# Kernel tuning notes

Measured on AMD Instinct MI355X. Metric: run time of the kernel, lower is better.

Reference implementation:

```python
import jax, jax.numpy as jnp
import numpy as np

EMBED_DIM = 1024
NUM_HEADS = 16
HEAD_DIM = EMBED_DIM // NUM_HEADS
SCALING = HEAD_DIM ** -0.5
TGT_LEN, BSZ = 2048, 2


def setup_inputs() -> dict:
    key = jax.random.key(0)
    k1, k2, k3 = jax.random.split(key, 3)
    return {
        "query": jax.random.normal(k1, (TGT_LEN, BSZ, EMBED_DIM), jnp.float32),
        "in_proj_weight": jax.random.normal(k2, (3 * EMBED_DIM, EMBED_DIM), jnp.float32) * (EMBED_DIM ** -0.5),
        "in_proj_bias": jnp.zeros((3 * EMBED_DIM,), jnp.float32),
        "out_w": jax.random.normal(k3, (EMBED_DIM, EMBED_DIM), jnp.float32) * (EMBED_DIM ** -0.5),
        "out_b": jnp.zeros((EMBED_DIM,), jnp.float32),
    }


def reference(query, in_proj_weight, in_proj_bias, out_w, out_b):
    tgt_len, bsz, embed_dim = query.shape
    # fused QKV projection (self-attention path: qkv_same)
    qkv = query @ in_proj_weight.T + in_proj_bias  # [T, B, 3E]
    q, k, v = jnp.split(qkv, 3, axis=-1)
    q = q * SCALING
    # [T, B, E] -> [B*H, T, hd]
    def to_heads(x):
        return x.reshape(tgt_len, bsz * NUM_HEADS, HEAD_DIM).transpose(1, 0, 2)
    q, k, v = to_heads(q), to_heads(k), to_heads(v)
    attn_weights = jnp.einsum('bqd,bkd->bqk', q, k)          # [B*H, T, T]
    attn_weights = jax.nn.softmax(attn_weights, axis=-1)
    attn = jnp.einsum('bqk,bkd->bqd', attn_weights, v)       # [B*H, T, hd]
    attn = attn.transpose(1, 0, 2).reshape(tgt_len, bsz, embed_dim)
    attn = attn @ out_w.T + out_b
    # averaged attention weights over heads (need_weights=True)
    avg_weights = attn_weights.reshape(bsz, NUM_HEADS, tgt_len, tgt_len).mean(axis=1)
    return attn, avg_weights
```

## Files before the change

kernel.cpp:

```cpp
#include <hip/hip_runtime.h>
#include <hip/hip_bf16.h>
#include <math.h>

#define T_LEN 2048
#define BSZ   2
#define EMB   1024
#define NH    16
#define HD    64
#define BHN   (BSZ*NH)
#define M1    (T_LEN*BSZ)
#define SCAL  0.125f
#define QSCALE (0.125f * 1.44269504088896f)

typedef __attribute__((ext_vector_type(8))) short bf16x8;
typedef __attribute__((ext_vector_type(4))) float f32x4;
typedef __attribute__((ext_vector_type(2))) unsigned int u32x2;

__device__ inline unsigned short f2bf(float x) {
    union { float f; unsigned u; } v; v.f = x;
    unsigned r = v.u + 0x7FFF + ((v.u >> 16) & 1);
    return (unsigned short)(r >> 16);
}

__device__ inline unsigned pack2bf(float a, float b) {
    union { __hip_bfloat162 h; unsigned u; } v;
    v.h = __float22bfloat162_rn(make_float2(a, b));
    return v.u;
}

__device__ inline float fexp2(float x) {
#if __has_builtin(__builtin_amdgcn_exp2f)
    return __builtin_amdgcn_exp2f(x);
#else
    return exp2f(x);
#endif
}

__device__ inline void async16(const unsigned short* g, unsigned short* l) {
    __builtin_amdgcn_global_load_lds(
        (const __attribute__((address_space(1))) void*)g,
        (__attribute__((address_space(3))) void*)l, 16, 0, 0);
}

__device__ inline void bar() {
    asm volatile("" ::: "memory");
    __builtin_amdgcn_s_barrier();
    asm volatile("" ::: "memory");
}

__device__ inline unsigned short* swz(unsigned short* base, int r, int c) {
    return base + (((r << 3) + (c ^ (r & 7))) << 3);
}
__device__ inline const unsigned short* swz(const unsigned short* base, int r, int c) {
    return base + (((r << 3) + (c ^ (r & 7))) << 3);
}

__device__ inline void xchg(unsigned e, unsigned o, unsigned& w_lo, unsigned& w_hi) {
#if __has_builtin(__builtin_amdgcn_permlane32_swap) && __has_builtin(__builtin_amdgcn_permlane16_swap)
    u32x2 x = __builtin_amdgcn_permlane32_swap(e, o, false, false);
    u32x2 y = __builtin_amdgcn_permlane16_swap(x[0], x[1], false, false);
    w_lo = y[0]; w_hi = y[1];
#else
    int lane = (int)(threadIdx.x & 63);
    int quad = lane >> 4, l16 = lane & 15;
    int srcA = ((quad & 1) * 2) * 16 + l16;
    int srcB = ((quad & 1) * 2 + 1) * 16 + l16;
    unsigned ea = (unsigned)__shfl((int)e, srcA, 64);
    unsigned oa = (unsigned)__shfl((int)o, srcA, 64);
    unsigned eb = (unsigned)__shfl((int)e, srcB, 64);
    unsigned ob = (unsigned)__shfl((int)o, srcB, 64);
    w_lo = (quad >> 1) ? oa : ea;
    w_hi = (quad >> 1) ? ob : eb;
#endif
}

__global__ __launch_bounds__(256) void cvt3_kernel(
    const float* __restrict__ s0, const float* __restrict__ s1,
    const float* __restrict__ s2, unsigned short* __restrict__ dst,
    int n0, int n1)
{
    int idx = blockIdx.x * 256 + threadIdx.x;
    const float* src; int o;
    if (idx < n0)           { src = s0; o = idx; }
    else if (idx < n0 + n1) { src = s1; o = idx - n0; }
    else                    { src = s2; o = idx - n0 - n1; }
    float4 a = reinterpret_cast<const float4*>(src)[(size_t)o * 2];
    float4 c = reinterpret_cast<const float4*>(src)[(size_t)o * 2 + 1];
    unsigned w[4] = { pack2bf(a.x, a.y), pack2bf(a.z, a.w),
                      pack2bf(c.x, c.y), pack2bf(c.z, c.w) };
    reinterpret_cast<uint4*>(dst)[idx] = *reinterpret_cast<uint4*>(w);
}

__global__ __launch_bounds__(256) void qkv_mfma_kernel(
    const unsigned short* __restrict__ A, const unsigned short* __restrict__ B,
    const float* __restrict__ bias,
    unsigned short* __restrict__ Q16, unsigned short* __restrict__ K16,
    unsigned short* __restrict__ Vt16)
{
    constexpr int BM = 128, BN = 128, BK = 32, K = 1024;
    __shared__ unsigned short As[BM * BK];
    __shared__ unsigned short Bs[BN * BK];
    const int tid = threadIdx.x;
    const int lane = tid & 63, wave = tid >> 6;
    const int quad = lane >> 4, l16 = lane & 15;
    const int wr = wave >> 1, wc = wave & 1;
    const int m0 = blockIdx.x * BM, n0 = blockIdx.y * BN;

    f32x4 zero4 = {0.f, 0.f, 0.f, 0.f};
    f32x4 acc[4][4];
    #pragma unroll
    for (int i = 0; i < 4; ++i)
        #pragma unroll
        for (int j = 0; j < 4; ++j) acc[i][j] = zero4;

    for (int k0 = 0; k0 < K; k0 += BK) {
        __syncthreads();
        #pragma unroll
        for (int t = 0; t < 2; ++t) {
            int c = t * 256 + tid;
            int m = c >> 2, kb = c & 3;
            async16(&A[(size_t)(m0 + m) * K + k0 + kb * 8], &As[c * 8]);
            async16(&B[(size_t)(n0 + m) * K + k0 + kb * 8], &Bs[c * 8]);
        }
        __syncthreads();
        bf16x8 af[4], bfr[4];
        #pragma unroll
        for (int i = 0; i < 4; ++i) {
            af[i]  = *reinterpret_cast<const bf16x8*>(&As[(wr * 64 + i * 16 + l16) * BK + quad * 8]);
            bfr[i] = *reinterpret_cast<const bf16x8*>(&Bs[(wc * 64 + i * 16 + l16) * BK + quad * 8]);
        }
        #pragma unroll
        for (int i = 0; i < 4; ++i)
            #pragma unroll
            for (int j = 0; j < 4; ++j)
                acc[i][j] = __builtin_amdgcn_mfma_f32_16x16x32_bf16(af[i], bfr[j], acc[i][j], 0, 0, 0);
    }

    #pragma unroll
    for (int j = 0; j < 4; ++j) {
        int n = n0 + wc * 64 + j * 16 + l16;
        float bv = bias[n];
        int which = n >> 10;
        int c = n & 1023;
        int h = c >> 6, d = c & 63;
        #pragma unroll
        for (int i = 0; i < 4; ++i) {
            #pragma unroll
            for (int r = 0; r < 4; ++r) {
                int m = m0 + wr * 64 + i * 16 + quad * 4 + r;
                int t = m >> 1, b = m & 1;
                int bh = b * NH + h;
                float v = acc[i][j][r] + bv;
                if (which == 0)      Q16[((size_t)bh * T_LEN + t) * HD + d] = f2bf(v * QSCALE);
                else if (which == 1) K16[((size_t)bh * T_LEN + t) * HD + d] = f2bf(v);
                else                 Vt16[((size_t)bh * HD + d) * T_LEN + t] = f2bf(v);
            }
        }
    }
}

__global__ __launch_bounds__(512, 4) void flash_mfma_kernel(
    const unsigned short* __restrict__ Qb, const unsigned short* __restrict__ Kb,
    const unsigned short* __restrict__ Vt, unsigned short* __restrict__ AO,
    float* __restrict__ Rrow)
{
    __shared__ unsigned short Ks[2][64 * 64];
    __shared__ unsigned short Vs[2][64 * 64];
    const int tid = threadIdx.x;
    const int lane = tid & 63, wave = tid >> 6;
    const int quad = lane >> 4, l16 = lane & 15;

    const int lin = blockIdx.y * gridDim.x + blockIdx.x;
    const int xcd = lin & 7, slot = lin >> 3;
    const int bh = xcd * 4 + (slot >> 4);
    const int qt = slot & 15;
    const int q0 = qt * 128;
    const int b = bh >> 4, h = bh & 15;

    const unsigned short* Qp =
        Qb + ((size_t)bh * T_LEN + q0 + wave * 16 + l16) * HD;
    bf16x8 qf0 = *reinterpret_cast<const bf16x8*>(Qp + quad * 8);
    bf16x8 qf1 = *reinterpret_cast<const bf16x8*>(Qp + 32 + quad * 8);

    f32x4 zero4 = {0.f, 0.f, 0.f, 0.f};
    f32x4 oacc[4] = {zero4, zero4, zero4, zero4};
    float l_part = 0.f;

    const unsigned short* Kbase = Kb + (size_t)bh * T_LEN * HD;
    const unsigned short* Vbase = Vt + (size_t)bh * HD * T_LEN;

    const int r0 = tid >> 3, c0 = (tid & 7) ^ (r0 & 7);

    async16(&Kbase[(size_t)r0 * HD + c0 * 8], &Ks[0][tid * 8]);
    async16(&Vbase[(size_t)r0 * T_LEN + c0 * 8], &Vs[0][tid * 8]);

    int cur = 0;
    for (int kt = 0; kt < T_LEN; kt += 64) {
        if (kt + 64 < T_LEN) {
            const int nb = cur ^ 1, nkt = kt + 64;
            async16(&Kbase[(size_t)(nkt + r0) * HD + c0 * 8], &Ks[nb][tid * 8]);
            async16(&Vbase[(size_t)r0 * T_LEN + nkt + c0 * 8], &Vs[nb][tid * 8]);
            asm volatile("s_waitcnt vmcnt(2)" ::: "memory");
        } else {
            asm volatile("s_waitcnt vmcnt(0)" ::: "memory");
        }
        bar();

        const unsigned short* Kt = Ks[cur];
        const unsigned short* Vv = Vs[cur];

        f32x4 sacc[4] = {zero4, zero4, zero4, zero4};
        __builtin_amdgcn_s_setprio(1);
        #pragma unroll
        for (int kb = 0; kb < 4; ++kb) {
            bf16x8 kf0 = *reinterpret_cast<const bf16x8*>(swz(Kt, kb * 16 + l16, quad));
            sacc[kb] = __builtin_amdgcn_mfma_f32_16x16x32_bf16(kf0, qf0, sacc[kb], 0, 0, 0);
            bf16x8 kf1 = *reinterpret_cast<const bf16x8*>(swz(Kt, kb * 16 + l16, 4 + quad));
            sacc[kb] = __builtin_amdgcn_mfma_f32_16x16x32_bf16(kf1, qf1, sacc[kb], 0, 0, 0);
        }
        __builtin_amdgcn_s_setprio(0);

        unsigned dlo[4], dhi[4];
        #pragma unroll
        for (int kb = 0; kb < 4; ++kb) {
            float p0 = fexp2(sacc[kb][0]);
            float p1 = fexp2(sacc[kb][1]);
            float p2 = fexp2(sacc[kb][2]);
            float p3 = fexp2(sacc[kb][3]);
            l_part += (p0 + p1) + (p2 + p3);
            dlo[kb] = pack2bf(p0, p1);
            dhi[kb] = pack2bf(p2, p3);
        }

        bf16x8 pfrag[2];
        #pragma unroll
        for (int ks = 0; ks < 2; ++ks) {
            unsigned w0, w1, w2, w3;
            xchg(dlo[2 * ks], dlo[2 * ks + 1], w0, w2);
            xchg(dhi[2 * ks], dhi[2 * ks + 1], w1, w3);
            union { bf16x8 v; unsigned u[4]; } P;
            P.u[0] = w0; P.u[1] = w1; P.u[2] = w2; P.u[3] = w3;
            pfrag[ks] = P.v;
        }

        __builtin_amdgcn_s_setprio(1);
        #pragma unroll
        for (int ks = 0; ks < 2; ++ks) {
            #pragma unroll
            for (int dt = 0; dt < 4; ++dt) {
                bf16x8 va = *reinterpret_cast<const bf16x8*>(swz(Vv, dt * 16 + l16, ks * 4 + quad));
                oacc[dt] = __builtin_amdgcn_mfma_f32_16x16x32_bf16(va, pfrag[ks], oacc[dt], 0, 0, 0);
            }
        }
        __builtin_amdgcn_s_setprio(0);

        bar();
        cur ^= 1;
    }

    l_part += __shfl_xor(l_part, 16);
    l_part += __shfl_xor(l_part, 32);
    float rl = 1.0f / l_part;
    int q = q0 + wave * 16 + l16;
    size_t base = ((size_t)q * BSZ + b) * EMB + h * HD;
    #pragma unroll
    for (int dt = 0; dt < 4; ++dt) {
        unsigned o[2] = { pack2bf(oacc[dt][0] * rl, oacc[dt][1] * rl),
                          pack2bf(oacc[dt][2] * rl, oacc[dt][3] * rl) };
        *reinterpret_cast<uint2*>(&AO[base + dt * 16 + quad * 4]) = *reinterpret_cast<uint2*>(o);
    }
    if (quad == 0)
        Rrow[(size_t)bh * T_LEN + q] = rl;
}

__global__ __launch_bounds__(256) void avg_mfma_kernel(
    const unsigned short* __restrict__ Qb, const unsigned short* __restrict__ Kb,
    const float* __restrict__ Rrow, float* __restrict__ avg_out)
{
    __shared__ unsigned short Ks[2][2][64 * 64];
    const int tid = threadIdx.x;
    const int lane = tid & 63, wave = tid >> 6;
    const int quad = lane >> 4, l16 = lane & 15;
    const int kt = blockIdx.x, qt = blockIdx.y, b = blockIdx.z;
    const int q0 = qt * 128, k0 = kt * 64;

    auto stage_pair = [&](int buf, int h0) {
        const unsigned short* Kg = Kb + ((size_t)(b * NH + h0) * T_LEN + k0) * HD;
        #pragma unroll
        for (int t = 0; t < 4; ++t) {
            int c = t * 256 + tid;
            int hh = c >> 9, cl = c & 511;
            int r = cl >> 3, cc = (cl & 7) ^ (r & 7);
            async16(&Kg[(size_t)hh * T_LEN * HD + (size_t)r * HD + cc * 8],
                    &Ks[buf][0][0] + (size_t)c * 8);
        }
    };

    f32x4 zero4 = {0.f, 0.f, 0.f, 0.f};
    f32x4 acc[2][4];
    #pragma unroll
    for (int s = 0; s < 2; ++s)
        #pragma unroll
        for (int c = 0; c < 4; ++c) acc[s][c] = zero4;

    stage_pair(0, 0);
    int cur = 0;
    for (int g = 0; g < NH / 2; ++g) {
        if (g + 1 < NH / 2) {
            stage_pair(cur ^ 1, 2 * (g + 1));
            asm volatile("s_waitcnt vmcnt(4)" ::: "memory");
        } else {
            asm volatile("s_waitcnt vmcnt(0)" ::: "memory");
        }
        bar();

        #pragma unroll
        for (int hh = 0; hh < 2; ++hh) {
            const int bh = b * NH + 2 * g + hh;
            const unsigned short* Kt = Ks[cur][hh];
            bf16x8 kf[4][2];
            #pragma unroll
            for (int c = 0; c < 4; ++c) {
                kf[c][0] = *reinterpret_cast<const bf16x8*>(swz(Kt, c * 16 + l16, quad));
                kf[c][1] = *reinterpret_cast<const bf16x8*>(swz(Kt, c * 16 + l16, 4 + quad));
            }
            #pragma unroll
            for (int s = 0; s < 2; ++s) {
                const int qrow = q0 + s * 64 + wave * 16;
                const unsigned short* Qp = Qb + ((size_t)bh * T_LEN + qrow + l16) * HD;
                bf16x8 qf0 = *reinterpret_cast<const bf16x8*>(Qp + quad * 8);
                bf16x8 qf1 = *reinterpret_cast<const bf16x8*>(Qp + 32 + quad * 8);
                float4 rlv = *reinterpret_cast<const float4*>(
                    &Rrow[(size_t)bh * T_LEN + qrow + quad * 4]);

                f32x4 sacc[4] = {zero4, zero4, zero4, zero4};
                __builtin_amdgcn_s_setprio(1);
                #pragma unroll
                for (int c = 0; c < 4; ++c) {
                    sacc[c] = __builtin_amdgcn_mfma_f32_16x16x32_bf16(qf0, kf[c][0], sacc[c], 0, 0, 0);
                    sacc[c] = __builtin_amdgcn_mfma_f32_16x16x32_bf16(qf1, kf[c][1], sacc[c], 0, 0, 0);
                }
                __builtin_amdgcn_s_setprio(0);

                float rl4[4] = { rlv.x, rlv.y, rlv.z, rlv.w };
                #pragma unroll
                for (int c = 0; c < 4; ++c)
                    #pragma unroll
                    for (int r = 0; r < 4; ++r)
                        acc[s][c][r] += fexp2(sacc[c][r]) * rl4[r];
            }
        }
        bar();
        cur ^= 1;
    }

    #pragma unroll
    for (int s = 0; s < 2; ++s)
        #pragma unroll
        for (int r = 0; r < 4; ++r) {
            int q = q0 + s * 64 + wave * 16 + quad * 4 + r;
            size_t base = ((size_t)b * T_LEN + q) * T_LEN + k0;
            #pragma unroll
            for (int c = 0; c < 4; ++c)
                avg_out[base + c * 16 + l16] = acc[s][c][r] * (1.0f / 16.0f);
        }
}

__global__ __launch_bounds__(256) void out_mfma_kernel(
    const unsigned short* __restrict__ A, const unsigned short* __restrict__ B,
    const float* __restrict__ bias, float* __restrict__ out)
{
    constexpr int BM = 128, BN = 128, BK = 32, K = 1024;
    __shared__ unsigned short As[BM * BK];
    __shared__ unsigned short Bs[BN * BK];
    const int tid = threadIdx.x;
    const int lane = tid & 63, wave = tid >> 6;
    const int quad = lane >> 4, l16 = lane & 15;
    const int wr = wave >> 1, wc = wave & 1;
    const int m0 = blockIdx.x * BM, n0 = blockIdx.y * BN;

    f32x4 zero4 = {0.f, 0.f, 0.f, 0.f};
    f32x4 acc[4][4];
    #pragma unroll
    for (int i = 0; i < 4; ++i)
        #pragma unroll
        for (int j = 0; j < 4; ++j) acc[i][j] = zero4;

    for (int k0 = 0; k0 < K; k0 += BK) {
        __syncthreads();
        #pragma unroll
        for (int t = 0; t < 2; ++t) {
            int c = t * 256 + tid;
            int m = c >> 2, kb = c & 3;
            async16(&A[(size_t)(m0 + m) * K + k0 + kb * 8], &As[c * 8]);
            async16(&B[(size_t)(n0 + m) * K + k0 + kb * 8], &Bs[c * 8]);
        }
        __syncthreads();
        bf16x8 af[4], bfr[4];
        #pragma unroll
        for (int i = 0; i < 4; ++i) {
            af[i]  = *reinterpret_cast<const bf16x8*>(&As[(wr * 64 + i * 16 + l16) * BK + quad * 8]);
            bfr[i] = *reinterpret_cast<const bf16x8*>(&Bs[(wc * 64 + i * 16 + l16) * BK + quad * 8]);
        }
        #pragma unroll
        for (int i = 0; i < 4; ++i)
            #pragma unroll
            for (int j = 0; j < 4; ++j)
                acc[i][j] = __builtin_amdgcn_mfma_f32_16x16x32_bf16(af[i], bfr[j], acc[i][j], 0, 0, 0);
    }

    #pragma unroll
    for (int j = 0; j < 4; ++j) {
        int n = n0 + wc * 64 + j * 16 + l16;
        float bv = bias[n];
        #pragma unroll
        for (int i = 0; i < 4; ++i) {
            #pragma unroll
            for (int r = 0; r < 4; ++r) {
                int m = m0 + wr * 64 + i * 16 + quad * 4 + r;
                out[(size_t)m * 1024 + n] = acc[i][j][r] + bv;
            }
        }
    }
}

extern "C" void kernel_launch(void* const* d_in, const int* in_sizes, int n_in,
                              void* d_out, int out_size, void* d_ws, size_t ws_size,
                              hipStream_t stream)
{
    const float* query = (const float*)d_in[0];
    const float* wqkv  = (const float*)d_in[1];
    const float* bqkv  = (const float*)d_in[2];
    const float* wout  = (const float*)d_in[3];
    const float* bout  = (const float*)d_in[4];
    float* out = (float*)d_out;

    char* ws = (char*)d_ws;
    const size_t E_Q   = (size_t)M1 * EMB;
    const size_t E_W   = (size_t)3 * EMB * EMB;
    const size_t E_WO  = (size_t)EMB * EMB;
    const size_t E_QKV = (size_t)BHN * T_LEN * HD;

    unsigned short* queryb = (unsigned short*)ws;
    unsigned short* wqkvb  = queryb + E_Q;
    unsigned short* woutb  = wqkvb + E_W;
    unsigned short* Q16    = woutb + E_WO;
    unsigned short* K16    = Q16 + E_QKV;
    unsigned short* Vt16   = K16 + E_QKV;
    unsigned short* AO16   = Vt16 + E_QKV;
    float* Lr = (float*)(AO16 + E_Q);
    const size_t need = (E_Q + E_W + E_WO + 4 * E_QKV) * 2 + (size_t)BHN * T_LEN * 4;
    if (ws_size < need) return;

    cvt3_kernel<<<(int)((E_Q + E_W + E_WO) / 8 / 256), 256, 0, stream>>>(
        query, wqkv, wout, queryb, (int)(E_Q / 8), (int)(E_W / 8));

    qkv_mfma_kernel<<<dim3(M1 / 128, 3072 / 128), 256, 0, stream>>>(queryb, wqkvb, bqkv, Q16, K16, Vt16);
    flash_mfma_kernel<<<dim3(T_LEN / 128, BHN), 512, 0, stream>>>(Q16, K16, Vt16, AO16, Lr);
    avg_mfma_kernel<<<dim3(T_LEN / 64, T_LEN / 128, BSZ), 256, 0, stream>>>(Q16, K16, Lr, out + (size_t)M1 * EMB);
    out_mfma_kernel<<<dim3(M1 / 128, 1024 / 128), 256, 0, stream>>>(AO16, woutb, bout, out);
}
```

Measured before the change: 242.3 us.

## Double K/V tile size in flash kernel and restructure avg kernel to 512 threads

The flash attention kernel now stages 128-key K and V tiles per iteration instead of 64, which halves the number of barriers and loop iterations and adds a 16-chunk swizzle for the wider V tile. The averaged-weights kernel moves to 512 threads with 128-key tiles. Each wave now owns 16 query rows across 8 key blocks instead of 32 rows across 4 blocks, so K fragments are read per pass rather than reused for two query sub-tiles. LDS use doubles in both kernels, which can lower occupancy, and register pressure rises from the wider score and accumulator arrays.

```diff
diff --git a/kernel.cpp b/kernel.cpp
--- a/kernel.cpp
+++ b/kernel.cpp
@@ -48,11 +48,11 @@
     asm volatile("" ::: "memory");
 }
 
-__device__ inline unsigned short* swz(unsigned short* base, int r, int c) {
-    return base + (((r << 3) + (c ^ (r & 7))) << 3);
-}
 __device__ inline const unsigned short* swz(const unsigned short* base, int r, int c) {
     return base + (((r << 3) + (c ^ (r & 7))) << 3);
+}
+__device__ inline const unsigned short* swz16(const unsigned short* base, int r, int c) {
+    return base + (((r << 4) + (c ^ (r & 7))) << 3);
 }
 
 __device__ inline void xchg(unsigned e, unsigned o, unsigned& w_lo, unsigned& w_hi) {
@@ -164,8 +164,8 @@
     const unsigned short* __restrict__ Vt, unsigned short* __restrict__ AO,
     float* __restrict__ Rrow)
 {
-    __shared__ unsigned short Ks[2][64 * 64];
-    __shared__ unsigned short Vs[2][64 * 64];
+    __shared__ unsigned short Ks[2][128 * 64];
+    __shared__ unsigned short Vs[2][64 * 128];
     const int tid = threadIdx.x;
     const int lane = tid & 63, wave = tid >> 6;
     const int quad = lane >> 4, l16 = lane & 15;
@@ -189,18 +189,26 @@
     const unsigned short* Kbase = Kb + (size_t)bh * T_LEN * HD;
     const unsigned short* Vbase = Vt + (size_t)bh * HD * T_LEN;
 
-    const int r0 = tid >> 3, c0 = (tid & 7) ^ (r0 & 7);
-
-    async16(&Kbase[(size_t)r0 * HD + c0 * 8], &Ks[0][tid * 8]);
-    async16(&Vbase[(size_t)r0 * T_LEN + c0 * 8], &Vs[0][tid * 8]);
+    const int ck0 = tid, ck1 = tid + 512;
+    const int kr0 = ck0 >> 3, kc0 = (ck0 & 7) ^ (kr0 & 7);
+    const int kr1 = ck1 >> 3, kc1 = (ck1 & 7) ^ (kr1 & 7);
+    const int vr0 = ck0 >> 4, vc0 = (ck0 & 15) ^ (vr0 & 7);
+    const int vr1 = ck1 >> 4, vc1 = (ck1 & 15) ^ (vr1 & 7);
+
+    auto stage = [&](int buf, int kt) {
+        async16(&Kbase[(size_t)(kt + kr0) * HD + kc0 * 8], &Ks[buf][ck0 * 8]);
+        async16(&Kbase[(size_t)(kt + kr1) * HD + kc1 * 8], &Ks[buf][ck1 * 8]);
+        async16(&Vbase[(size_t)vr0 * T_LEN + kt + vc0 * 8], &Vs[buf][ck0 * 8]);
+        async16(&Vbase[(size_t)vr1 * T_LEN + kt + vc1 * 8], &Vs[buf][ck1 * 8]);
+    };
+
+    stage(0, 0);
 
     int cur = 0;
-    for (int kt = 0; kt < T_LEN; kt += 64) {
-        if (kt + 64 < T_LEN) {
-            const int nb = cur ^ 1, nkt = kt + 64;
-            async16(&Kbase[(size_t)(nkt + r0) * HD + c0 * 8], &Ks[nb][tid * 8]);
-            async16(&Vbase[(size_t)r0 * T_LEN + nkt + c0 * 8], &Vs[nb][tid * 8]);
-            asm volatile("s_waitcnt vmcnt(2)" ::: "memory");
+    for (int kt = 0; kt < T_LEN; kt += 128) {
+        if (kt + 128 < T_LEN) {
+            stage(cur ^ 1, kt + 128);
+            asm volatile("s_waitcnt vmcnt(4)" ::: "memory");
         } else {
             asm volatile("s_waitcnt vmcnt(0)" ::: "memory");
         }
@@ -209,47 +217,44 @@
         const unsigned short* Kt = Ks[cur];
         const unsigned short* Vv = Vs[cur];
 
-        f32x4 sacc[4] = {zero4, zero4, zero4, zero4};
+        unsigned dlo[8], dhi[8];
+        #pragma unroll
+        for (int half = 0; half < 2; ++half) {
+            f32x4 sacc[4] = {zero4, zero4, zero4, zero4};
+            __builtin_amdgcn_s_setprio(1);
+            #pragma unroll
+            for (int j = 0; j < 4; ++j) {
+                int kb = half * 4 + j;
+                bf16x8 kf0 = *reinterpret_cast<const bf16x8*>(swz(Kt, kb * 16 + l16, quad));
+                sacc[j] = __builtin_amdgcn_mfma_f32_16x16x32_bf16(kf0, qf0, sacc[j], 0, 0, 0);
+                bf16x8 kf1 = *reinterpret_cast<const bf16x8*>(swz(Kt, kb * 16 + l16, 4 + quad));
+                sacc[j] = __builtin_amdgcn_mfma_f32_16x16x32_bf16(kf1, qf1, sacc[j], 0, 0, 0);
+            }
+            __builtin_amdgcn_s_setprio(0);
+            #pragma unroll
+            for (int j = 0; j < 4; ++j) {
+                float p0 = fexp2(sacc[j][0]);
+                float p1 = fexp2(sacc[j][1]);
+                float p2 = fexp2(sacc[j][2]);
+                float p3 = fexp2(sacc[j][3]);
+                l_part += (p0 + p1) + (p2 + p3);
+                dlo[half * 4 + j] = pack2bf(p0, p1);
+                dhi[half * 4 + j] = pack2bf(p2, p3);
+            }
+        }
+
         __builtin_amdgcn_s_setprio(1);
         #pragma unroll
-        for (int kb = 0; kb < 4; ++kb) {
-            bf16x8 kf0 = *reinterpret_cast<const bf16x8*>(swz(Kt, kb * 16 + l16, quad));
-            sacc[kb] = __builtin_amdgcn_mfma_f32_16x16x32_bf16(kf0, qf0, sacc[kb], 0, 0, 0);
-            bf16x8 kf1 = *reinterpret_cast<const bf16x8*>(swz(Kt, kb * 16 + l16, 4 + quad));
-            sacc[kb] = __builtin_amdgcn_mfma_f32_16x16x32_bf16(kf1, qf1, sacc[kb], 0, 0, 0);
-        }
-        __builtin_amdgcn_s_setprio(0);
-
-        unsigned dlo[4], dhi[4];
-        #pragma unroll
-        for (int kb = 0; kb < 4; ++kb) {
-            float p0 = fexp2(sacc[kb][0]);
-            float p1 = fexp2(sacc[kb][1]);
-            float p2 = fexp2(sacc[kb][2]);
-            float p3 = fexp2(sacc[kb][3]);
-            l_part += (p0 + p1) + (p2 + p3);
-            dlo[kb] = pack2bf(p0, p1);
-            dhi[kb] = pack2bf(p2, p3);
-        }
-
-        bf16x8 pfrag[2];
-        #pragma unroll
-        for (int ks = 0; ks < 2; ++ks) {
+        for (int ks = 0; ks < 4; ++ks) {
             unsigned w0, w1, w2, w3;
             xchg(dlo[2 * ks], dlo[2 * ks + 1], w0, w2);
             xchg(dhi[2 * ks], dhi[2 * ks + 1], w1, w3);
             union { bf16x8 v; unsigned u[4]; } P;
             P.u[0] = w0; P.u[1] = w1; P.u[2] = w2; P.u[3] = w3;
-            pfrag[ks] = P.v;
-        }
-
-        __builtin_amdgcn_s_setprio(1);
-        #pragma unroll
-        for (int ks = 0; ks < 2; ++ks) {
             #pragma unroll
             for (int dt = 0; dt < 4; ++dt) {
-                bf16x8 va = *reinterpret_cast<const bf16x8*>(swz(Vv, dt * 16 + l16, ks * 4 + quad));
-                oacc[dt] = __builtin_amdgcn_mfma_f32_16x16x32_bf16(va, pfrag[ks], oacc[dt], 0, 0, 0);
+                bf16x8 va = *reinterpret_cast<const bf16x8*>(swz16(Vv, dt * 16 + l16, ks * 4 + quad));
+                oacc[dt] = __builtin_amdgcn_mfma_f32_16x16x32_bf16(va, P.v, oacc[dt], 0, 0, 0);
             }
         }
         __builtin_amdgcn_s_setprio(0);
@@ -273,23 +278,23 @@
         Rrow[(size_t)bh * T_LEN + q] = rl;
 }
 
-__global__ __launch_bounds__(256) void avg_mfma_kernel(
+__global__ __launch_bounds__(512, 4) void avg_mfma_kernel(
     const unsigned short* __restrict__ Qb, const unsigned short* __restrict__ Kb,
     const float* __restrict__ Rrow, float* __restrict__ avg_out)
 {
-    __shared__ unsigned short Ks[2][2][64 * 64];
+    __shared__ unsigned short Ks[2][2][128 * 64];
     const int tid = threadIdx.x;
     const int lane = tid & 63, wave = tid >> 6;
     const int quad = lane >> 4, l16 = lane & 15;
     const int kt = blockIdx.x, qt = blockIdx.y, b = blockIdx.z;
-    const int q0 = qt * 128, k0 = kt * 64;
+    const int q0 = qt * 128, k0 = kt * 128;
 
     auto stage_pair = [&](int buf, int h0) {
         const unsigned short* Kg = Kb + ((size_t)(b * NH + h0) * T_LEN + k0) * HD;
         #pragma unroll
         for (int t = 0; t < 4; ++t) {
-            int c = t * 256 + tid;
-            int hh = c >> 9, cl = c & 511;
+            int c = t * 512 + tid;
+            int hh = c >> 10, cl = c & 1023;
             int r = cl >> 3, cc = (cl & 7) ^ (r & 7);
             async16(&Kg[(size_t)hh * T_LEN * HD + (size_t)r * HD + cc * 8],
                     &Ks[buf][0][0] + (size_t)c * 8);
@@ -297,11 +302,9 @@
     };
 
     f32x4 zero4 = {0.f, 0.f, 0.f, 0.f};
-    f32x4 acc[2][4];
-    #pragma unroll
-    for (int s = 0; s < 2; ++s)
-        #pragma unroll
-        for (int c = 0; c < 4; ++c) acc[s][c] = zero4;
+    f32x4 acc[8];
+    #pragma unroll
+    for (int kb = 0; kb < 8; ++kb) acc[kb] = zero4;
 
     stage_pair(0, 0);
     int cur = 0;
@@ -318,52 +321,44 @@
         for (int hh = 0; hh < 2; ++hh) {
             const int bh = b * NH + 2 * g + hh;
             const unsigned short* Kt = Ks[cur][hh];
-            bf16x8 kf[4][2];
-            #pragma unroll
-            for (int c = 0; c < 4; ++c) {
-                kf[c][0] = *reinterpret_cast<const bf16x8*>(swz(Kt, c * 16 + l16, quad));
-                kf[c][1] = *reinterpret_cast<const bf16x8*>(swz(Kt, c * 16 + l16, 4 + quad));
-            }
-            #pragma unroll
-            for (int s = 0; s < 2; ++s) {
-                const int qrow = q0 + s * 64 + wave * 16;
-                const unsigned short* Qp = Qb + ((size_t)bh * T_LEN + qrow + l16) * HD;
-                bf16x8 qf0 = *reinterpret_cast<const bf16x8*>(Qp + quad * 8);
-                bf16x8 qf1 = *reinterpret_cast<const bf16x8*>(Qp + 32 + quad * 8);
-                float4 rlv = *reinterpret_cast<const float4*>(
-                    &Rrow[(size_t)bh * T_LEN + qrow + quad * 4]);
-
-                f32x4 sacc[4] = {zero4, zero4, zero4, zero4};
-                __builtin_amdgcn_s_setprio(1);
+            const int qrow = q0 + wave * 16;
+            const unsigned short* Qp = Qb + ((size_t)bh * T_LEN + qrow + l16) * HD;
+            bf16x8 qf0 = *reinterpret_cast<const bf16x8*>(Qp + quad * 8);
+            bf16x8 qf1 = *reinterpret_cast<const bf16x8*>(Qp + 32 + quad * 8);
+            float4 rlv = *reinterpret_cast<const float4*>(
+                &Rrow[(size_t)bh * T_LEN + qrow + quad * 4]);
+
+            f32x4 sacc[8];
+            __builtin_amdgcn_s_setprio(1);
+            #pragma unroll
+            for (int kb = 0; kb < 8; ++kb) {
+                sacc[kb] = zero4;
+                bf16x8 kf0 = *reinterpret_cast<const bf16x8*>(swz(Kt, kb * 16 + l16, quad));
+                sacc[kb] = __builtin_amdgcn_mfma_f32_16x16x32_bf16(qf0, kf0, sacc[kb], 0, 0, 0);
+                bf16x8 kf1 = *reinterpret_cast<const bf16x8*>(swz(Kt, kb * 16 + l16, 4 + quad));
+                sacc[kb] = __builtin_amdgcn_mfma_f32_16x16x32_bf16(qf1, kf1, sacc[kb], 0, 0, 0);
+            }
+            __builtin_amdgcn_s_setprio(0);
+
+            float rl4[4] = { rlv.x, rlv.y, rlv.z, rlv.w };
+            #pragma unroll
+            for (int kb = 0; kb < 8; ++kb)
                 #pragma unroll
-                for (int c = 0; c < 4; ++c) {
-                    sacc[c] = __builtin_amdgcn_mfma_f32_16x16x32_bf16(qf0, kf[c][0], sacc[c], 0, 0, 0);
-                    sacc[c] = __builtin_amdgcn_mfma_f32_16x16x32_bf16(qf1, kf[c][1], sacc[c], 0, 0, 0);
-                }
-                __builtin_amdgcn_s_setprio(0);
-
-                float rl4[4] = { rlv.x, rlv.y, rlv.z, rlv.w };
-                #pragma unroll
-                for (int c = 0; c < 4; ++c)
-                    #pragma unroll
-                    for (int r = 0; r < 4; ++r)
-                        acc[s][c][r] += fexp2(sacc[c][r]) * rl4[r];
-            }
+                for (int r = 0; r < 4; ++r)
+                    acc[kb][r] += fexp2(sacc[kb][r]) * rl4[r];
         }
         bar();
         cur ^= 1;
     }
 
     #pragma unroll
-    for (int s = 0; s < 2; ++s)
-        #pragma unroll
-        for (int r = 0; r < 4; ++r) {
-            int q = q0 + s * 64 + wave * 16 + quad * 4 + r;
-            size_t base = ((size_t)b * T_LEN + q) * T_LEN + k0;
-            #pragma unroll
-            for (int c = 0; c < 4; ++c)
-                avg_out[base + c * 16 + l16] = acc[s][c][r] * (1.0f / 16.0f);
-        }
+    for (int r = 0; r < 4; ++r) {
+        int q = q0 + wave * 16 + quad * 4 + r;
+        size_t base = ((size_t)b * T_LEN + q) * T_LEN + k0;
+        #pragma unroll
+        for (int kb = 0; kb < 8; ++kb)
+            avg_out[base + kb * 16 + l16] = acc[kb][r] * (1.0f / 16.0f);
+    }
 }
 
 __global__ __launch_bounds__(256) void out_mfma_kernel(
@@ -457,6 +452,6 @@
 
     qkv_mfma_kernel<<<dim3(M1 / 128, 3072 / 128), 256, 0, stream>>>(queryb, wqkvb, bqkv, Q16, K16, Vt16);
     flash_mfma_kernel<<<dim3(T_LEN / 128, BHN), 512, 0, stream>>>(Q16, K16, Vt16, AO16, Lr);
-    avg_mfma_kernel<<<dim3(T_LEN / 64, T_LEN / 128, BSZ), 256, 0, stream>>>(Q16, K16, Lr, out + (size_t)M1 * EMB);
+    avg_mfma_kernel<<<dim3(T_LEN / 128, T_LEN / 128, BSZ), 512, 0, stream>>>(Q16, K16, Lr, out + (size_t)M1 * EMB);
     out_mfma_kernel<<<dim3(M1 / 128, 1024 / 128), 256, 0, stream>>>(AO16, woutb, bout, out);
 }
```

After: 263.3 us. 1.09x slower.
